# Kernel optimization log

Hardware: AMD Instinct MI355X
Metric: run time of the kernel (lower is better)

Reference implementation:

```python
import jax, jax.numpy as jnp
import numpy as np

N_NODES = 48758
REL_NUM = 5
BN_EPS = 1e-5


def _dan(h, edge_index, edge_type, win_w, win_b, wrel, cout_w, cout_b):
    # One DAN layer: gather -> gcn-norm scatter-sum + per-relation transform -> scatter-softmax -> scatter-sum.
    dst, src = edge_index[0], edge_index[1]
    xlin = h @ win_w + win_b                         # [N, D]
    x_j = xlin[src]                                  # [E, D] per-edge gather
    # gcn_norm(edge_index, add_self_loops=False): deg over col (= edge_index[1])
    ones = jnp.ones(src.shape[0], xlin.dtype)
    deg = jax.ops.segment_sum(ones, src, num_segments=N_NODES)
    dis = jnp.where(deg > 0, 1.0 / jnp.sqrt(deg), 0.0)
    norm = dis[dst] * dis[src]                       # [E]
    msg_gcn = jax.ops.segment_sum(x_j * norm[:, None], dst, num_segments=N_NODES)
    # per-relation linear transform on edge messages (small fixed relation loop)
    res = jnp.zeros_like(x_j)
    for r in range(REL_NUM):
        res = res + jnp.where((edge_type == r)[:, None], x_j @ wrel[r], 0.0)
    # scatter-softmax over destination-node neighborhoods, per feature channel
    m = jax.ops.segment_max(res, dst, num_segments=N_NODES)      # [N, D]
    e = jnp.exp(res - m[dst])
    s = jax.ops.segment_sum(e, dst, num_segments=N_NODES)
    weig = e / s[dst]
    msg = jax.ops.segment_sum(res * weig, dst, num_segments=N_NODES)
    return (msg_gcn + 0.1 * jax.nn.relu(msg)) @ cout_w + cout_b


def setup_inputs() -> dict:
    key = jax.random.key(0)
    ks = jax.random.split(key, 18)
    D = 128
    E = 750000
    s = 0.05
    inp = {}
    inp['x'] = jax.random.normal(ks[0], (N_NODES, D), jnp.float32)
    inp['edge_index'] = jax.random.randint(ks[1], (2, E), 0, N_NODES)
    inp['edge_type'] = jax.random.randint(ks[2], (E,), 0, REL_NUM)
    inp['edge_weight'] = jax.random.uniform(ks[3], (E,), jnp.float32)
    inp['idx'] = jax.random.randint(ks[4], (4096,), 0, N_NODES)
    # input projection + batchnorm params
    inp['proj_w'] = jax.random.normal(ks[5], (D, D), jnp.float32) * s
    inp['proj_b'] = jnp.zeros((D,), jnp.float32)
    inp['bn_g'] = jnp.ones((D,), jnp.float32)
    inp['bn_b'] = jnp.zeros((D,), jnp.float32)
    # two DAN layers (hidden=output=128)
    inp['win0_w'] = jax.random.normal(ks[6], (D, D), jnp.float32) * s
    inp['win0_b'] = jnp.zeros((D,), jnp.float32)
    inp['wrel0'] = jax.random.normal(ks[7], (REL_NUM, D, D), jnp.float32) * s
    inp['cout0_w'] = jax.random.normal(ks[8], (D, D), jnp.float32) * s
    inp['cout0_b'] = jnp.zeros((D,), jnp.float32)
    inp['win1_w'] = jax.random.normal(ks[9], (D, D), jnp.float32) * s
    inp['win1_b'] = jnp.zeros((D,), jnp.float32)
    inp['wrel1'] = jax.random.normal(ks[10], (REL_NUM, D, D), jnp.float32) * s
    inp['cout1_w'] = jax.random.normal(ks[11], (D, D), jnp.float32) * s
    inp['cout1_b'] = jnp.zeros((D,), jnp.float32)
    return inp


def reference(x, edge_index, edge_type, edge_weight, idx,
              proj_w, proj_b, bn_g, bn_b,
              win0_w, win0_b, wrel0, cout0_w, cout0_b,
              win1_w, win1_b, wrel1, cout1_w, cout1_b):
    # proj -> BatchNorm1d (training-mode batch stats) -> relu
    h = x @ proj_w + proj_b
    mu = jnp.mean(h, axis=0)
    var = jnp.mean(jnp.square(h - mu), axis=0)
    h = (h - mu) / jnp.sqrt(var + BN_EPS) * bn_g + bn_b
    h = jax.nn.relu(h)
    h = _dan(h, edge_index, edge_type, win0_w, win0_b, wrel0, cout0_w, cout0_b)
    h = _dan(h, edge_index, edge_type, win1_w, win1_b, wrel1, cout1_w, cout1_b)
    h = jax.nn.gelu(h, approximate=False)  # dropout is identity for reference
    return h[idx]
```

## Files before the change

### kernel.cpp

```cpp
#include <hip/hip_runtime.h>

#define HIST_BPG 32
#define HIST_B   (HIST_BPG * 4)
#define HIST_MAXW 12288

__device__ inline float bf2f(unsigned short u) {
    return __uint_as_float(((unsigned)u) << 16);
}
__device__ inline unsigned short f2bf(float f) {
    unsigned u = __float_as_uint(f);
    u += 0x7fffu + ((u >> 16) & 1u);
    return (unsigned short)(u >> 16);
}

__device__ inline int xcd_swizzle(int bid, int n)
{
    const int NX = 8;
    int q = n / NX, r = n % NX;
    int xcd = bid % NX;
    int rank = bid / NX;
    return (xcd < r) ? xcd * (q + 1) + rank : r * (q + 1) + (xcd - r) * q + rank;
}

typedef __attribute__((ext_vector_type(8))) short short8v;
typedef __attribute__((ext_vector_type(4))) float f32x4;


__device__ __forceinline__
void gemmf32_body(const float* __restrict__ A, const float* __restrict__ W,
                  const float* __restrict__ bias, float* __restrict__ C,
                  unsigned short* __restrict__ Ct, int M, int tile)
{
    __shared__ float As[64][132];
    __shared__ float Ws[32][128];

    const int tid = threadIdx.x;
    const int row0 = tile * 64;

#pragma unroll
    for (int i = 0; i < 8; ++i) {
        int idx = tid + i * 256;
        int rr = idx >> 5;
        int cc = (idx & 31) << 2;
        int gr = row0 + rr;
        float4 v = make_float4(0.f, 0.f, 0.f, 0.f);
        if (gr < M) v = *reinterpret_cast<const float4*>(A + (size_t)gr * 128 + cc);
        *reinterpret_cast<float4*>(&As[rr][cc]) = v;
    }

    const int tx = tid & 15;
    const int ty = tid >> 4;
    float acc[4][8];
#pragma unroll
    for (int i = 0; i < 4; ++i)
#pragma unroll
        for (int j = 0; j < 8; ++j) acc[i][j] = 0.f;

    for (int kt = 0; kt < 4; ++kt) {
        __syncthreads();
#pragma unroll
        for (int i = 0; i < 4; ++i) {
            int idx = tid + i * 256;
            int rr = idx >> 5;
            int cc = (idx & 31) << 2;
            *reinterpret_cast<float4*>(&Ws[rr][cc]) =
                *reinterpret_cast<const float4*>(W + (size_t)(kt * 32 + rr) * 128 + cc);
        }
        __syncthreads();
#pragma unroll
        for (int kk = 0; kk < 32; ++kk) {
            const int k = kt * 32 + kk;
            float a0 = As[ty * 4 + 0][k];
            float a1 = As[ty * 4 + 1][k];
            float a2 = As[ty * 4 + 2][k];
            float a3 = As[ty * 4 + 3][k];
            float w[8];
#pragma unroll
            for (int j = 0; j < 8; ++j) w[j] = Ws[kk][tx + 16 * j];
#pragma unroll
            for (int j = 0; j < 8; ++j) {
                acc[0][j] = fmaf(a0, w[j], acc[0][j]);
                acc[1][j] = fmaf(a1, w[j], acc[1][j]);
                acc[2][j] = fmaf(a2, w[j], acc[2][j]);
                acc[3][j] = fmaf(a3, w[j], acc[3][j]);
            }
        }
    }

    float bb[8];
#pragma unroll
    for (int j = 0; j < 8; ++j) bb[j] = bias ? bias[tx + 16 * j] : 0.f;

#pragma unroll
    for (int i = 0; i < 4; ++i) {
        int gr = row0 + ty * 4 + i;
        if (gr >= M) continue;
#pragma unroll
        for (int j = 0; j < 8; ++j) {
            float v = acc[i][j] + bb[j];
            if (C)  C[(size_t)gr * 128 + tx + 16 * j] = v;
            if (Ct) Ct[(size_t)(tx + 16 * j) * 128 + gr] = f2bf(v);
        }
    }
}

__device__ __forceinline__
void mfmaw_body(const unsigned short* __restrict__ A,
                const unsigned short* __restrict__ Wmat,
                const float* __restrict__ bias,
                float* __restrict__ Cf, unsigned short* __restrict__ Cb,
                int M, int tile)
{
    __shared__ unsigned short Bs[16384];

    const int tid = threadIdx.x;
#pragma unroll
    for (int i = 0; i < 4; ++i) {
        int idx = tid + i * 512;
        uint4 v = *reinterpret_cast<const uint4*>(Wmat + (size_t)idx * 8);
        int row = idx >> 4;
        int j = idx & 15;
        int byte = row * 256 + ((j ^ (row & 15)) << 4);
        *reinterpret_cast<uint4*>(reinterpret_cast<char*>(Bs) + byte) = v;
    }

    const int wave = tid >> 6;
    const int lane = tid & 63;
    const int grp = lane >> 4;
    const int l16 = lane & 15;
    const int row = tile * 128 + wave * 16 + l16;
    const int rc = row < M ? row : M - 1;

    short8v a[4];
#pragma unroll
    for (int kt = 0; kt < 4; ++kt)
        a[kt] = *reinterpret_cast<const short8v*>(A + (size_t)rc * 128 + kt * 32 + grp * 8);

    __syncthreads();

    f32x4 acc[8] = {};
#pragma unroll
    for (int kt = 0; kt < 4; ++kt) {
        const int joff = kt * 4 + grp;
#pragma unroll
        for (int n = 0; n < 8; ++n) {
            int brow = 16 * n + l16;
            int byte = brow * 256 + ((joff ^ (brow & 15)) << 4);
            short8v b = *reinterpret_cast<const short8v*>(
                reinterpret_cast<const char*>(Bs) + byte);
            acc[n] = __builtin_amdgcn_mfma_f32_16x16x32_bf16(b, a[kt], acc[n], 0, 0, 0);
        }
    }

    if (row >= M) return;

    float4 bb[8];
#pragma unroll
    for (int n = 0; n < 8; ++n)
        bb[n] = bias ? *reinterpret_cast<const float4*>(bias + 16 * n + grp * 4)
                     : make_float4(0.f, 0.f, 0.f, 0.f);

#pragma unroll
    for (int n = 0; n < 8; ++n) {
        float v0 = acc[n][0] + bb[n].x;
        float v1 = acc[n][1] + bb[n].y;
        float v2 = acc[n][2] + bb[n].z;
        float v3 = acc[n][3] + bb[n].w;
        if (Cf) {
            *reinterpret_cast<float4*>(Cf + (size_t)row * 128 + 16 * n + grp * 4) =
                make_float4(v0, v1, v2, v3);
        }
        if (Cb) {
            unsigned u0 = (unsigned)f2bf(v0) | ((unsigned)f2bf(v1) << 16);
            unsigned u1 = (unsigned)f2bf(v2) | ((unsigned)f2bf(v3) << 16);
            *reinterpret_cast<uint2*>(Cb + (size_t)row * 128 + 16 * n + grp * 4) =
                make_uint2(u0, u1);
        }
    }
}

__device__ void fused_dispatch(const unsigned short* A, const unsigned short* Wt,
                               const float* biasbuf, unsigned short* Xb,
                               unsigned short* Yb, int base, int M, int nmats,
                               int bid, int nF)
{
    int w = xcd_swizzle(bid, nF);
    int m = w % nmats;
    int tile = w / nmats;
    unsigned short* out = (m == 0) ? Xb : Yb + (size_t)(m - 1) * (size_t)M * 128;
    mfmaw_body(A, Wt + (size_t)(base + m) * 16384,
               biasbuf + (size_t)(base + m) * 128, nullptr, out, M, tile);
}

__device__ void biasprod_body(const float* __restrict__ v, const float* __restrict__ W,
                              const float* __restrict__ add, float* __restrict__ out)
{
    int t = threadIdx.x;
    if (t >= 128) return;
    float s = add ? add[t] : 0.f;
    for (int j = 0; j < 128; ++j) s = fmaf(v[j], W[(size_t)j * 128 + t], s);
    out[t] = s;
}

__device__ void wtconv_body(const float* __restrict__ W, unsigned short* __restrict__ O)
{
    for (int i = threadIdx.x; i < 16384; i += 256) {
        int k = i >> 7, n = i & 127;
        O[(size_t)n * 128 + k] = f2bf(W[i]);
    }
}

__device__ void bn_stats_body(const float* __restrict__ h, float* __restrict__ sums,
                              int Nn, int b)
{
    const int c = threadIdx.x & 127;
    const int half = threadIdx.x >> 7;
    float s = 0.f, q = 0.f;
    for (int row = b * 2 + half; row < Nn; row += 512) {
        float v = h[(size_t)row * 128 + c];
        s += v;
        q += v * v;
    }
    __shared__ float ls[256], lq[256];
    ls[threadIdx.x] = s;
    lq[threadIdx.x] = q;
    __syncthreads();
    if (half == 0) {
        s += ls[threadIdx.x + 128];
        q += lq[threadIdx.x + 128];
        atomicAdd(&sums[c], s);
        atomicAdd(&sums[128 + c], q);
    }
}

__device__ void scan_block_sums_body(const int* __restrict__ cnt, int* __restrict__ bsum,
                                     int Nn, int b)
{
    __shared__ int sd[256];
    int tid = threadIdx.x;
    int i = b * 256 + tid;
    sd[tid] = i < Nn ? ((cnt[i] + 3) & ~3) : 0;
    __syncthreads();
#pragma unroll
    for (int s = 128; s > 0; s >>= 1) {
        if (tid < s) sd[tid] += sd[tid + s];
        __syncthreads();
    }
    if (tid == 0) bsum[b] = sd[0];
}

__device__ void scan_offsets_body(int* __restrict__ bsum, int nb)
{
    __shared__ int sd[256];
    int tid = threadIdx.x;
    int v = tid < nb ? bsum[tid] : 0;
    sd[tid] = v;
    __syncthreads();
    for (int d = 1; d < 256; d <<= 1) {
        int t = tid >= d ? sd[tid - d] : 0;
        __syncthreads();
        sd[tid] += t;
        __syncthreads();
    }
    if (tid < nb) bsum[tid] = sd[tid] - v;
}


__global__ __launch_bounds__(256)
void hist_kernel(const int* __restrict__ ei, unsigned* __restrict__ partial,
                 int Nn, int E, int WORDS, int HALFR)
{
    __shared__ unsigned sh[HIST_MAXW];
    const int hbid = blockIdx.x;
    const int g = hbid / HIST_BPG;
    const int j = hbid - g * HIST_BPG;

    for (int w = threadIdx.x; w < WORDS; w += 256) sh[w] = 0;
    __syncthreads();

    const int* col = (g < 2) ? (ei + E) : ei;
    const int base = (g & 1) * HALFR;
    const size_t e0 = (size_t)E * j / HIST_BPG;
    const size_t e1 = (size_t)E * (j + 1) / HIST_BPG;
    for (size_t e = e0 + threadIdx.x; e < e1; e += 256) {
        int n = col[e] - base;
        if ((unsigned)n < (unsigned)HALFR)
            atomicAdd(&sh[n >> 1], 1u << ((n & 1) * 16));
    }
    __syncthreads();

    unsigned* out = partial + (size_t)hbid * WORDS;
    for (int w = threadIdx.x; w < WORDS; w += 256) out[w] = sh[w];
}

__global__ __launch_bounds__(256)
void kprod1(const float* win0w, const float* win0b, const float* win1w, const float* win1b,
            const float* cout0w, const float* cout0b, const float* cout1w,
            const float* cout1b, const float* wrel0,
            float* WfA1, unsigned short* Wt, float* biasbuf, int nrel)
{
    const int IA1 = 1 + nrel, IC1 = 2 + 2 * nrel;
    const int nProd = 1 + nrel;
    int bid = blockIdx.x;
    if (bid < 2 * nProd) {
        int p = bid >> 1, tile = bid & 1;
        if (p == 0)
            gemmf32_body(cout0w, win1w, nullptr, WfA1, Wt + (size_t)IA1 * 16384, 128, tile);
        else
            gemmf32_body(win0w, wrel0 + (size_t)(p - 1) * 16384, nullptr,
                         nullptr, Wt + (size_t)p * 16384, 128, tile);
        return;
    }
    bid -= 2 * nProd;
    if (bid < nProd) {
        if (bid == 0) biasprod_body(cout0b, win1w, win1b, biasbuf + (size_t)IA1 * 128);
        else biasprod_body(win0b, wrel0 + (size_t)(bid - 1) * 16384, nullptr,
                           biasbuf + (size_t)bid * 128);
        return;
    }
    bid -= nProd;
    if (bid == 0) { wtconv_body(win0w, Wt); return; }
    if (bid == 1) { wtconv_body(cout1w, Wt + (size_t)IC1 * 16384); return; }
    int t = threadIdx.x;
    if (t < 128) {
        biasbuf[t] = win0b[t];
        biasbuf[(size_t)IC1 * 128 + t] = cout1b[t];
    }
}

__global__ __launch_bounds__(256)
void kmid(const float* wrel1, const float* WfA1, unsigned short* Wt, float* biasbuf,
          const float* x, const float* proj_w, const float* proj_b, float* h,
          int M, int nrel)
{
    const int IA1 = 1 + nrel, IB1 = 2 + nrel;
    int bid = blockIdx.x;
    if (bid < 2 * nrel) {
        int p = bid >> 1, tile = bid & 1;
        gemmf32_body(WfA1, wrel1 + (size_t)p * 16384, nullptr,
                     nullptr, Wt + (size_t)(IB1 + p) * 16384, 128, tile);
        return;
    }
    bid -= 2 * nrel;
    if (bid < nrel) {
        biasprod_body(biasbuf + (size_t)IA1 * 128, wrel1 + (size_t)bid * 16384, nullptr,
                      biasbuf + (size_t)(IB1 + bid) * 128);
        return;
    }
    bid -= nrel;
    gemmf32_body(x, proj_w, proj_b, h, nullptr, M, bid);
}

__global__ __launch_bounds__(256)
void k2_reduce_bnstats(const unsigned* __restrict__ partial, float* __restrict__ dis,
                       int* __restrict__ cnt, const float* __restrict__ h,
                       float* __restrict__ bnsums, int Nn, int WORDS, int HALFR, int nRed)
{
    int bid = blockIdx.x;
    if (bid < nRed) {
        int t = bid * 256 + threadIdx.x;
        if (t < 4 * WORDS) {
            int histo = t / (2 * WORDS);
            int rem = t - histo * 2 * WORDS;
            int half = rem / WORDS;
            int w = rem - half * WORDS;
            int g = histo * 2 + half;
            unsigned slo = 0, shi = 0;
            const unsigned* p = partial + (size_t)(g * HIST_BPG) * WORDS + w;
#pragma unroll 4
            for (int j = 0; j < HIST_BPG; ++j) {
                unsigned u = p[(size_t)j * WORDS];
                slo += u & 0xffffu;
                shi += u >> 16;
            }
            int n0 = half * HALFR + 2 * w;
            int n1 = n0 + 1;
            if (histo == 0) {
                if (n0 < Nn) dis[n0] = slo ? rsqrtf((float)slo) : 0.f;
                if (n1 < Nn) dis[n1] = shi ? rsqrtf((float)shi) : 0.f;
            } else {
                if (n0 < Nn) cnt[n0] = (int)slo;
                if (n1 < Nn) cnt[n1] = (int)shi;
            }
        }
        return;
    }
    bn_stats_body(h, bnsums, Nn, bid - nRed);
}

__global__ __launch_bounds__(256)
void k3_bnfin_scan1(const float* __restrict__ sums, const float* __restrict__ g,
                    const float* __restrict__ b, float* __restrict__ sc,
                    const int* __restrict__ cnt, int* __restrict__ bsum, int Nn)
{
    if (blockIdx.x == 0) {
        int c = threadIdx.x;
        if (c < 128) {
            float inv = 1.f / (float)Nn;
            float mu = sums[c] * inv;
            float var = sums[128 + c] * inv - mu * mu;
            float rstd = rsqrtf(var + 1e-5f);
            float scale = rstd * g[c];
            sc[c] = scale;
            sc[128 + c] = b[c] - mu * scale;
        }
        return;
    }
    scan_block_sums_body(cnt, bsum, Nn, blockIdx.x - 1);
}

__global__ __launch_bounds__(256)
void k4_scanoff_bnapply(int* __restrict__ bsum, int nb,
                        const float* __restrict__ h, const float* __restrict__ sc,
                        unsigned short* __restrict__ hb, size_t n4)
{
    if (blockIdx.x == 0) { scan_offsets_body(bsum, nb); return; }
    size_t i = (size_t)(blockIdx.x - 1) * 256 + threadIdx.x;
    if (i >= n4) return;
    int c = (int)(i & 31) << 2;
    float4 v = reinterpret_cast<const float4*>(h)[i];
    float o0 = fmaxf(fmaf(v.x, sc[c + 0], sc[128 + c + 0]), 0.f);
    float o1 = fmaxf(fmaf(v.y, sc[c + 1], sc[128 + c + 1]), 0.f);
    float o2 = fmaxf(fmaf(v.z, sc[c + 2], sc[128 + c + 2]), 0.f);
    float o3 = fmaxf(fmaf(v.w, sc[c + 3], sc[128 + c + 3]), 0.f);
    ushort4 pk = make_ushort4(f2bf(o0), f2bf(o1), f2bf(o2), f2bf(o3));
    reinterpret_cast<ushort4*>(hb)[i] = pk;
}

__global__ __launch_bounds__(256)
void k4b_scanfinal(const int* __restrict__ cnt, const int* __restrict__ bsum,
                   int* __restrict__ rowptr, int* __restrict__ cursor,
                   uint4* __restrict__ csr, unsigned* __restrict__ Yw,
                   unsigned sink_woff, int Nn, int nb)
{
    if ((int)blockIdx.x == nb) {
        int t = threadIdx.x;
        if (t < 64) Yw[sink_woff + t] = 0xC2C8C2C8u;
        return;
    }
    __shared__ int sd[256];
    int tid = threadIdx.x;
    int b = blockIdx.x;
    int i = b * 256 + tid;
    int v = i < Nn ? cnt[i] : 0;
    int pv = (v + 3) & ~3;
    sd[tid] = pv;
    __syncthreads();
    for (int d = 1; d < 256; d <<= 1) {
        int t2 = tid >= d ? sd[tid - d] : 0;
        __syncthreads();
        sd[tid] += t2;
        __syncthreads();
    }
    if (i < Nn) {
        int off = sd[tid] - pv + bsum[b];
        rowptr[i] = off;
        cursor[i] = off;
        uint4 sink = make_uint4(0u, sink_woff, 0u, 0u);
        for (int j = v; j < pv; ++j) csr[off + j] = sink;
        if (i == Nn - 1) {
            rowptr[Nn] = off + pv;
            for (int q = 0; q < 8; ++q) csr[off + pv + q] = sink;
        }
    }
}

__global__ __launch_bounds__(512)
void k5_mfma_scatter(const unsigned short* hb, const unsigned short* Wt,
                     const float* biasbuf, unsigned short* Xb, unsigned short* Yb,
                     int M, int nmats, int nF,
                     const int* __restrict__ ei, const int* __restrict__ et,
                     const float* __restrict__ dis, int* __restrict__ cursor,
                     uint4* __restrict__ csr, int E, int Nn, int nS)
{
    const int minv = nF < nS ? nF : nS;
    int bid = blockIdx.x;
    int fIdx = -1, sIdx = -1;
    if (bid < 2 * minv) {
        if (bid & 1) fIdx = bid >> 1; else sIdx = bid >> 1;
    } else {
        int rem = bid - 2 * minv;
        if (nF > nS) fIdx = minv + rem; else sIdx = minv + rem;
    }
    if (sIdx >= 0) {
        int e = sIdx * 512 + threadIdx.x;
        if (e < E) {
            int dst = ei[e];
            int src = ei[E + e];
            int pos = atomicAdd(&cursor[dst], 1);
            float nrm = dis[dst] * dis[src];
            csr[pos] = make_uint4((unsigned)(src * 64),
                                  (unsigned)((et[e] * Nn + src) * 64),
                                  __float_as_uint(nrm), 0u);
        }
        return;
    }
    fused_dispatch(hb, Wt, biasbuf, Xb, Yb, 0, M, nmats, fIdx, nF);
}

__global__ __launch_bounds__(512)
void k_fusedpass(const unsigned short* A, const unsigned short* Wt, const float* biasbuf,
                 unsigned short* Xb, unsigned short* Yb, int base, int M, int nmats,
                 int nF)
{
    fused_dispatch(A, Wt, biasbuf, Xb, Yb, base, M, nmats, blockIdx.x, nF);
}

__global__ __launch_bounds__(512)
void k_cout_gelu(const unsigned short* __restrict__ A, const unsigned short* Wt,
                 const float* biasbuf, float* __restrict__ out, int mat, int M)
{
    const unsigned short* Wmat = Wt + (size_t)mat * 16384;
    const float* bias = biasbuf + (size_t)mat * 128;

    __shared__ unsigned short Bs[16384];
    const int tid = threadIdx.x;
#pragma unroll
    for (int i = 0; i < 4; ++i) {
        int idx = tid + i * 512;
        uint4 v = *reinterpret_cast<const uint4*>(Wmat + (size_t)idx * 8);
        int row = idx >> 4;
        int j = idx & 15;
        int byte = row * 256 + ((j ^ (row & 15)) << 4);
        *reinterpret_cast<uint4*>(reinterpret_cast<char*>(Bs) + byte) = v;
    }

    const int wave = tid >> 6;
    const int lane = tid & 63;
    const int grp = lane >> 4;
    const int l16 = lane & 15;
    const int row = blockIdx.x * 128 + wave * 16 + l16;
    const int rc = row < M ? row : M - 1;

    short8v a[4];
#pragma unroll
    for (int kt = 0; kt < 4; ++kt)
        a[kt] = *reinterpret_cast<const short8v*>(A + (size_t)rc * 128 + kt * 32 + grp * 8);

    __syncthreads();

    f32x4 acc[8] = {};
#pragma unroll
    for (int kt = 0; kt < 4; ++kt) {
        const int joff = kt * 4 + grp;
#pragma unroll
        for (int n = 0; n < 8; ++n) {
            int brow = 16 * n + l16;
            int byte = brow * 256 + ((joff ^ (brow & 15)) << 4);
            short8v b = *reinterpret_cast<const short8v*>(
                reinterpret_cast<const char*>(Bs) + byte);
            acc[n] = __builtin_amdgcn_mfma_f32_16x16x32_bf16(b, a[kt], acc[n], 0, 0, 0);
        }
    }

    if (row >= M) return;

    const float kg = 0.7071067811865475f;
#pragma unroll
    for (int n = 0; n < 8; ++n) {
        float4 bb = *reinterpret_cast<const float4*>(bias + 16 * n + grp * 4);
        float v0 = acc[n][0] + bb.x;
        float v1 = acc[n][1] + bb.y;
        float v2 = acc[n][2] + bb.z;
        float v3 = acc[n][3] + bb.w;
        v0 = 0.5f * v0 * (1.f + erff(v0 * kg));
        v1 = 0.5f * v1 * (1.f + erff(v1 * kg));
        v2 = 0.5f * v2 * (1.f + erff(v2 * kg));
        v3 = 0.5f * v3 * (1.f + erff(v3 * kg));
        *reinterpret_cast<float4*>(out + (size_t)row * 128 + 16 * n + grp * 4) =
            make_float4(v0, v1, v2, v3);
    }
}

__global__ __launch_bounds__(256)
void node_gather(const int* __restrict__ rowptr, const uint4* __restrict__ csr,
                 const unsigned* __restrict__ Xw, const unsigned* __restrict__ Yw,
                 unsigned short* __restrict__ outb,
                 const int* __restrict__ idxmap, int count)
{
    int gid = blockIdx.x * 4 + (threadIdx.x >> 6);
    if (gid >= count) return;
    int node = idxmap ? idxmap[gid] : gid;
    int lane = threadIdx.x & 63;

    int i = rowptr[node];
    const int end = rowptr[node + 1];

    float mg0 = 0.f, mg1 = 0.f, s0 = 0.f, s1 = 0.f, t0 = 0.f, t1 = 0.f;

    if (i < end) {
        uint4 cur[4];
#pragma unroll
        for (int q = 0; q < 4; ++q) cur[q] = csr[i + q];

        for (; i < end; i += 4) {
            uint4 nxt[4];
#pragma unroll
            for (int q = 0; q < 4; ++q) nxt[q] = csr[i + 4 + q];

            unsigned xp[4], yp[4];
#pragma unroll
            for (int q = 0; q < 4; ++q) {
                xp[q] = Xw[cur[q].x + lane];
                yp[q] = Yw[cur[q].y + lane];
            }
#pragma unroll
            for (int q = 0; q < 4; ++q) {
                float nrm = __uint_as_float(cur[q].z);
                float x0 = bf2f((unsigned short)(xp[q] & 0xffffu));
                float x1 = bf2f((unsigned short)(xp[q] >> 16));
                float y0 = bf2f((unsigned short)(yp[q] & 0xffffu));
                float y1 = bf2f((unsigned short)(yp[q] >> 16));
                float w0 = __expf(y0), w1 = __expf(y1);
                mg0 = fmaf(x0, nrm, mg0);
                mg1 = fmaf(x1, nrm, mg1);
                s0 += w0; s1 += w1;
                t0 = fmaf(y0, w0, t0);
                t1 = fmaf(y1, w1, t1);
            }
#pragma unroll
            for (int q = 0; q < 4; ++q) cur[q] = nxt[q];
        }
    }

    float o0 = mg0 + 0.1f * fmaxf(s0 > 0.f ? t0 / s0 : 0.f, 0.f);
    float o1 = mg1 + 0.1f * fmaxf(s1 > 0.f ? t1 / s1 : 0.f, 0.f);
    unsigned pk = (unsigned)f2bf(o0) | ((unsigned)f2bf(o1) << 16);
    *reinterpret_cast<unsigned*>(outb + (size_t)gid * 128 + (lane << 1)) = pk;
}

extern "C" void kernel_launch(void* const* d_in, const int* in_sizes, int n_in,
                              void* d_out, int out_size, void* d_ws, size_t ws_size,
                              hipStream_t stream)
{
    const float* x      = (const float*)d_in[0];
    const int*   ei     = (const int*)d_in[1];
    const int*   et     = (const int*)d_in[2];
    const int*   idxp   = (const int*)d_in[4];
    const float* proj_w = (const float*)d_in[5];
    const float* proj_b = (const float*)d_in[6];
    const float* bn_g   = (const float*)d_in[7];
    const float* bn_b   = (const float*)d_in[8];
    const float* win_w[2]  = {(const float*)d_in[9],  (const float*)d_in[14]};
    const float* win_b[2]  = {(const float*)d_in[10], (const float*)d_in[15]};
    const float* wrel[2]   = {(const float*)d_in[11], (const float*)d_in[16]};
    const float* cout_w[2] = {(const float*)d_in[12], (const float*)d_in[17]};
    const float* cout_b[2] = {(const float*)d_in[13], (const float*)d_in[18]};

    const int Nn  = in_sizes[0] / 128;
    const int E   = in_sizes[1] / 2;
    const int Mo  = in_sizes[4];
    const int nrel = in_sizes[11] / (128 * 128);
    const size_t ND = (size_t)Nn * 128;

    const int HALFR = ((Nn + 3) / 4) * 2;
    const int WORDS = HALFR / 2;
    if (WORDS > HIST_MAXW) return;

    const int IA1 = 1 + nrel;
    const int IC1 = 2 + 2 * nrel;
    const int NMATS = 3 + 2 * nrel;

    char* p = (char*)d_ws;
    float* h    = (float*)p;                  p += ND * 4;
    unsigned short* hb = (unsigned short*)p;  p += ND * 2;
    unsigned short* Xb = (unsigned short*)p;  p += ND * 2;
    unsigned short* Yb = (unsigned short*)p;  p += (size_t)nrel * ND * 2 + 256;
    unsigned short* msgb = (unsigned short*)p; p += ND * 2;
    unsigned short* Wt = (unsigned short*)p;  p += (size_t)NMATS * 16384 * 2;
    float* WfA1 = (float*)p;                  p += (size_t)16384 * 4;
    float* biasbuf = (float*)p;               p += (size_t)NMATS * 128 * 4;
    uint4* csr  = (uint4*)p;                  p += ((size_t)E + 3 * (size_t)Nn + 16) * 16;
    unsigned* partial = (unsigned*)p;         p += (size_t)HIST_B * WORDS * 4;
    float* dis  = (float*)p;                  p += (size_t)Nn * 4;
    int*   cnt  = (int*)p;                    p += (size_t)Nn * 4;
    int*   rowptr = (int*)p;                  p += ((size_t)Nn + 1) * 4;
    int*   cursor = (int*)p;                  p += (size_t)Nn * 4;
    int*   bsum = (int*)p;                    p += 1024 * 4;
    float* bnsums = (float*)p;                p += 256 * 4;
    float* bnsc   = (float*)p;                p += 256 * 4;
    if ((size_t)(p - (char*)d_ws) > ws_size) return;

    const unsigned sink_woff = (unsigned)((size_t)nrel * Nn * 64);

    const int gemmGrid = (Nn + 63) / 64;
    const int tiles128 = (Nn + 127) / 128;
    const size_t n4 = ND / 4;
    const int n4grid = (int)((n4 + 255) / 256);
    const int nb = (Nn + 255) / 256;
    const int nRed = (4 * WORDS + 255) / 256;
    const int nS = (E + 511) / 512;
    const int nmats = 1 + nrel;
    const int nFused = nmats * tiles128;

    hipMemsetAsync(bnsums, 0, 256 * 4, stream);

    hist_kernel<<<HIST_B, 256, 0, stream>>>(ei, partial, Nn, E, WORDS, HALFR);

    kprod1<<<2 * (1 + nrel) + (1 + nrel) + 3, 256, 0, stream>>>(
        win_w[0], win_b[0], win_w[1], win_b[1], cout_w[0], cout_b[0],
        cout_w[1], cout_b[1], wrel[0], WfA1, Wt, biasbuf, nrel);

    kmid<<<3 * nrel + gemmGrid, 256, 0, stream>>>(
        wrel[1], WfA1, Wt, biasbuf, x, proj_w, proj_b, h, Nn, nrel);

    k2_reduce_bnstats<<<nRed + 256, 256, 0, stream>>>(
        partial, dis, cnt, h, bnsums, Nn, WORDS, HALFR, nRed);

    k3_bnfin_scan1<<<1 + nb, 256, 0, stream>>>(bnsums, bn_g, bn_b, bnsc, cnt, bsum, Nn);

    k4_scanoff_bnapply<<<1 + n4grid, 256, 0, stream>>>(bsum, nb, h, bnsc, hb, n4);

    k4b_scanfinal<<<nb + 1, 256, 0, stream>>>(cnt, bsum, rowptr, cursor, csr,
                                              (unsigned*)Yb, sink_woff, Nn, nb);

    k5_mfma_scatter<<<nFused + nS, 512, 0, stream>>>(
        hb, Wt, biasbuf, Xb, Yb, Nn, nmats, nFused,
        ei, et, dis, cursor, csr, E, Nn, nS);

    node_gather<<<(Nn + 3) / 4, 256, 0, stream>>>(
        rowptr, csr, (const unsigned*)Xb, (const unsigned*)Yb, msgb, nullptr, Nn);

    k_fusedpass<<<nFused, 512, 0, stream>>>(msgb, Wt, biasbuf, Xb, Yb, IA1, Nn,
                                            nmats, nFused);

    node_gather<<<(Mo + 3) / 4, 256, 0, stream>>>(
        rowptr, csr, (const unsigned*)Xb, (const unsigned*)Yb, msgb, idxp, Mo);

    k_cout_gelu<<<(Mo + 127) / 128, 512, 0, stream>>>(
        msgb, Wt, biasbuf, (float*)d_out, IC1, Mo);
}
```

Before: 310.0 us.

## Run input projection as bf16 MFMA GEMM and move weight products off critical path

The fp32 input projection GEMM in kmid is replaced by converting x and proj_w to bf16 in kprod1 and running a dedicated MFMA kernel (kproj). The layer-1 weight-product GEMMs that shared kmid are moved into the later scan/BN-finalize kernel so they no longer delay the projection. This cuts the cost of the fp32 SIMT GEMM over all nodes but adds a bf16 conversion pass over x and rounds the projection input to bf16, which slightly reduces precision before batchnorm.

```diff
diff --git a/kernel.cpp b/kernel.cpp
--- a/kernel.cpp
+++ b/kernel.cpp
@@ -297,9 +297,11 @@
 void kprod1(const float* win0w, const float* win0b, const float* win1w, const float* win1b,
             const float* cout0w, const float* cout0b, const float* cout1w,
             const float* cout1b, const float* wrel0,
-            float* WfA1, unsigned short* Wt, float* biasbuf, int nrel)
-{
-    const int IA1 = 1 + nrel, IC1 = 2 + 2 * nrel;
+            const float* x, const float* proj_w, const float* proj_b,
+            unsigned short* xb, float* WfA1, unsigned short* Wt, float* biasbuf,
+            int nrel, size_t nx4)
+{
+    const int IA1 = 1 + nrel, IC1 = 2 + 2 * nrel, IPRJ = 3 + 2 * nrel;
     const int nProd = 1 + nrel;
     int bid = blockIdx.x;
     if (bid < 2 * nProd) {
@@ -321,34 +323,30 @@
     bid -= nProd;
     if (bid == 0) { wtconv_body(win0w, Wt); return; }
     if (bid == 1) { wtconv_body(cout1w, Wt + (size_t)IC1 * 16384); return; }
-    int t = threadIdx.x;
-    if (t < 128) {
-        biasbuf[t] = win0b[t];
-        biasbuf[(size_t)IC1 * 128 + t] = cout1b[t];
-    }
-}
-
-__global__ __launch_bounds__(256)
-void kmid(const float* wrel1, const float* WfA1, unsigned short* Wt, float* biasbuf,
-          const float* x, const float* proj_w, const float* proj_b, float* h,
-          int M, int nrel)
-{
-    const int IA1 = 1 + nrel, IB1 = 2 + nrel;
-    int bid = blockIdx.x;
-    if (bid < 2 * nrel) {
-        int p = bid >> 1, tile = bid & 1;
-        gemmf32_body(WfA1, wrel1 + (size_t)p * 16384, nullptr,
-                     nullptr, Wt + (size_t)(IB1 + p) * 16384, 128, tile);
-        return;
-    }
-    bid -= 2 * nrel;
-    if (bid < nrel) {
-        biasprod_body(biasbuf + (size_t)IA1 * 128, wrel1 + (size_t)bid * 16384, nullptr,
-                      biasbuf + (size_t)(IB1 + bid) * 128);
-        return;
-    }
-    bid -= nrel;
-    gemmf32_body(x, proj_w, proj_b, h, nullptr, M, bid);
+    if (bid == 2) { wtconv_body(proj_w, Wt + (size_t)IPRJ * 16384); return; }
+    if (bid == 3) {
+        int t = threadIdx.x;
+        if (t < 128) {
+            biasbuf[t] = win0b[t];
+            biasbuf[(size_t)IC1 * 128 + t] = cout1b[t];
+            biasbuf[(size_t)IPRJ * 128 + t] = proj_b[t];
+        }
+        return;
+    }
+    size_t i = (size_t)(bid - 4) * 256 + threadIdx.x;
+    if (i < nx4) {
+        float4 v = reinterpret_cast<const float4*>(x)[i];
+        ushort4 pk = make_ushort4(f2bf(v.x), f2bf(v.y), f2bf(v.z), f2bf(v.w));
+        reinterpret_cast<ushort4*>(xb)[i] = pk;
+    }
+}
+
+__global__ __launch_bounds__(512)
+void kproj(const unsigned short* xb, const unsigned short* Wt, const float* biasbuf,
+           float* h, int mat, int M)
+{
+    mfmaw_body(xb, Wt + (size_t)mat * 16384, biasbuf + (size_t)mat * 128,
+               h, nullptr, M, blockIdx.x);
 }
 
 __global__ __launch_bounds__(256)
@@ -389,11 +387,28 @@
 }
 
 __global__ __launch_bounds__(256)
-void k3_bnfin_scan1(const float* __restrict__ sums, const float* __restrict__ g,
-                    const float* __restrict__ b, float* __restrict__ sc,
-                    const int* __restrict__ cnt, int* __restrict__ bsum, int Nn)
-{
-    if (blockIdx.x == 0) {
+void k3_prod2_bnfin_scan1(const float* wrel1, const float* WfA1,
+                          unsigned short* Wt, float* biasbuf, int nrel,
+                          const float* __restrict__ sums, const float* __restrict__ g,
+                          const float* __restrict__ b, float* __restrict__ sc,
+                          const int* __restrict__ cnt, int* __restrict__ bsum, int Nn)
+{
+    const int IA1 = 1 + nrel, IB1 = 2 + nrel;
+    int bid = blockIdx.x;
+    if (bid < 2 * nrel) {
+        int p = bid >> 1, tile = bid & 1;
+        gemmf32_body(WfA1, wrel1 + (size_t)p * 16384, nullptr,
+                     nullptr, Wt + (size_t)(IB1 + p) * 16384, 128, tile);
+        return;
+    }
+    bid -= 2 * nrel;
+    if (bid < nrel) {
+        biasprod_body(biasbuf + (size_t)IA1 * 128, wrel1 + (size_t)bid * 16384, nullptr,
+                      biasbuf + (size_t)(IB1 + bid) * 128);
+        return;
+    }
+    bid -= nrel;
+    if (bid == 0) {
         int c = threadIdx.x;
         if (c < 128) {
             float inv = 1.f / (float)Nn;
@@ -406,7 +421,7 @@
         }
         return;
     }
-    scan_block_sums_body(cnt, bsum, Nn, blockIdx.x - 1);
+    scan_block_sums_body(cnt, bsum, Nn, bid - 1);
 }
 
 __global__ __launch_bounds__(256)
@@ -659,11 +674,13 @@
 
     const int IA1 = 1 + nrel;
     const int IC1 = 2 + 2 * nrel;
-    const int NMATS = 3 + 2 * nrel;
+    const int IPRJ = 3 + 2 * nrel;
+    const int NMATS = 4 + 2 * nrel;
 
     char* p = (char*)d_ws;
     float* h    = (float*)p;                  p += ND * 4;
     unsigned short* hb = (unsigned short*)p;  p += ND * 2;
+    unsigned short* xb = (unsigned short*)p;  p += ND * 2;
     unsigned short* Xb = (unsigned short*)p;  p += ND * 2;
     unsigned short* Yb = (unsigned short*)p;  p += (size_t)nrel * ND * 2 + 256;
     unsigned short* msgb = (unsigned short*)p; p += ND * 2;
@@ -683,7 +700,6 @@
 
     const unsigned sink_woff = (unsigned)((size_t)nrel * Nn * 64);
 
-    const int gemmGrid = (Nn + 63) / 64;
     const int tiles128 = (Nn + 127) / 128;
     const size_t n4 = ND / 4;
     const int n4grid = (int)((n4 + 255) / 256);
@@ -692,22 +708,25 @@
     const int nS = (E + 511) / 512;
     const int nmats = 1 + nrel;
     const int nFused = nmats * tiles128;
+    const int nConv = (int)((n4 + 255) / 256);
 
     hipMemsetAsync(bnsums, 0, 256 * 4, stream);
 
     hist_kernel<<<HIST_B, 256, 0, stream>>>(ei, partial, Nn, E, WORDS, HALFR);
 
-    kprod1<<<2 * (1 + nrel) + (1 + nrel) + 3, 256, 0, stream>>>(
+    kprod1<<<2 * (1 + nrel) + (1 + nrel) + 4 + nConv, 256, 0, stream>>>(
         win_w[0], win_b[0], win_w[1], win_b[1], cout_w[0], cout_b[0],
-        cout_w[1], cout_b[1], wrel[0], WfA1, Wt, biasbuf, nrel);
-
-    kmid<<<3 * nrel + gemmGrid, 256, 0, stream>>>(
-        wrel[1], WfA1, Wt, biasbuf, x, proj_w, proj_b, h, Nn, nrel);
+        cout_w[1], cout_b[1], wrel[0], x, proj_w, proj_b,
+        xb, WfA1, Wt, biasbuf, nrel, n4);
+
+    kproj<<<tiles128, 512, 0, stream>>>(xb, Wt, biasbuf, h, IPRJ, Nn);
 
     k2_reduce_bnstats<<<nRed + 256, 256, 0, stream>>>(
         partial, dis, cnt, h, bnsums, Nn, WORDS, HALFR, nRed);
 
-    k3_bnfin_scan1<<<1 + nb, 256, 0, stream>>>(bnsums, bn_g, bn_b, bnsc, cnt, bsum, Nn);
+    k3_prod2_bnfin_scan1<<<3 * nrel + 1 + nb, 256, 0, stream>>>(
+        wrel[1], WfA1, Wt, biasbuf, nrel,
+        bnsums, bn_g, bn_b, bnsc, cnt, bsum, Nn);
 
     k4_scanoff_bnapply<<<1 + n4grid, 256, 0, stream>>>(bsum, nb, h, bnsc, hb, n4);
 
```

New measurement: 291.9 us (median of 2 runs). 1.06x faster.
